# Performance work log

Measured on AMD Instinct MI355X. Metric: run time of the kernel, lower is better.

Reference implementation:

```python
import jax, jax.numpy as jnp
import numpy as np
import math

B, CIN, COUT, K, SD, H, W = 16, 512, 512, 3, 512, 32, 32


def setup_inputs() -> dict:
    key = jax.random.key(0)
    ks = jax.random.split(key, 7)
    return {
        "x": jax.random.normal(ks[0], (B, CIN, H, W), jnp.float32),
        "style": jax.random.normal(ks[1], (B, SD), jnp.float32),
        "noise": jax.random.normal(ks[2], (B, 1, H, W), jnp.float32),
        "weight": jax.random.normal(ks[3], (COUT, CIN, K, K), jnp.float32),
        "mod_w": jax.random.normal(ks[4], (CIN, SD), jnp.float32),
        "mod_b": jnp.ones((CIN,), jnp.float32),
        "noise_weight": jax.random.normal(ks[5], (1,), jnp.float32) * 0.1,
        "act_bias": jax.random.normal(ks[6], (COUT,), jnp.float32) * 0.1,
    }


def reference(x, style, noise, weight, mod_w, mod_b, noise_weight, act_bias):
    conv_scale = 1.0 / math.sqrt(CIN * K * K)  # equalized-lr scale of ModulatedConv2d
    mod_scale = 1.0 / math.sqrt(SD)            # EqualLinear scale (lr_mul=1)

    # style modulation: EqualLinear(style_dim -> in_channel), bias init 1
    s = style @ (mod_w.T * mod_scale) + mod_b              # [B, CIN]

    # per-sample modulated weights [B, COUT, CIN, K, K]
    w = conv_scale * weight[None] * s[:, None, :, None, None]

    # demodulation
    demod = jax.lax.rsqrt(jnp.sum(w * w, axis=(2, 3, 4)) + 1e-8)  # [B, COUT]
    w = w * demod[:, :, None, None, None]

    # grouped (per-sample) conv: vmap a single-sample conv over the batch
    pad = K // 2

    def conv1(xi, wi):
        return jax.lax.conv_general_dilated(
            xi[None], wi, window_strides=(1, 1),
            padding=[(pad, pad), (pad, pad)],
            dimension_numbers=("NCHW", "OIHW", "NCHW"))[0]

    out = jax.vmap(conv1)(x, w)  # [B, COUT, H, W]

    # NoiseInjection: out + weight * noise (scalar learned weight)
    out = out + noise_weight[0] * noise

    # FusedLeakyReLU: leaky_relu(out + bias, 0.2) * sqrt(2)
    out = jax.nn.leaky_relu(out + act_bias[None, :, None, None], 0.2) * math.sqrt(2.0)
    return out
```

## Files before the change

### kernel.cpp

```cpp
#include <hip/hip_runtime.h>
#include <cstdint>
#include <cstddef>

typedef unsigned short u16;
typedef __attribute__((ext_vector_type(8))) short short8;
typedef __attribute__((ext_vector_type(4))) float f32x4;

#define CIN   512
#define COUT  512
#define BATCH 16
#define HWSZ  1024
#define PADW  34

static constexpr float MOD_SCALE  = 0.044194173824159216f;
static constexpr float CONV_SCALE = 0.014731391274719739f;

#define WS_S    0
#define WS_DSC  (32*1024)
#define WS_WSQ  (64*1024)
#define WS_WBT  (64*1024 + 1024*1024)
#define WS_XSP  (WS_WBT + 9*512*512*2)

__device__ __forceinline__ u16 f2bf(float f) {
  union { float f; uint32_t u; } v; v.f = f;
  uint32_t r = v.u + 0x7fffu + ((v.u >> 16) & 1u);
  return (u16)(r >> 16);
}

__device__ __forceinline__ void gload16(const void* g, void* l) {
  __builtin_amdgcn_global_load_lds(
      (const __attribute__((address_space(1))) void*)g,
      (__attribute__((address_space(3))) void*)l, 16, 0, 0);
}

__global__ void k_style(const float* __restrict__ style, const float* __restrict__ mod_w,
                        const float* __restrict__ mod_b, float* __restrict__ s_out) {
  int gid  = blockIdx.x * blockDim.x + threadIdx.x;
  int w    = gid >> 6, lane = gid & 63;
  int b    = w >> 9, i = w & 511;
  const float4* st = (const float4*)(style + (size_t)b * 512);
  const float4* mw = (const float4*)(mod_w + (size_t)i * 512);
  float4 a0 = st[lane * 2], a1 = st[lane * 2 + 1];
  float4 w0 = mw[lane * 2], w1 = mw[lane * 2 + 1];
  float acc = a0.x*w0.x + a0.y*w0.y + a0.z*w0.z + a0.w*w0.w
            + a1.x*w1.x + a1.y*w1.y + a1.z*w1.z + a1.w*w1.w;
  #pragma unroll
  for (int off = 32; off; off >>= 1) acc += __shfl_xor(acc, off);
  if (lane == 0) s_out[w] = acc * MOD_SCALE + mod_b[i];
}

__global__ void k_wprep(const float* __restrict__ w, float* __restrict__ wsq,
                        u16* __restrict__ wbt) {
  int idx = blockIdx.x * 256 + threadIdx.x;
  const float* p = w + (size_t)idx * 9;
  float a = 0.f;
  #pragma unroll
  for (int kxy = 0; kxy < 9; ++kxy) {
    float v = p[kxy];
    a += v * v;
    wbt[(size_t)kxy * 262144 + idx] = f2bf(v);
  }
  wsq[idx] = a;
}

__global__ void k_dscale(const float* __restrict__ wsq, const float* __restrict__ s,
                         float* __restrict__ dsc) {
  int gid  = blockIdx.x * blockDim.x + threadIdx.x;
  int w    = gid >> 6, lane = gid & 63;
  int b    = w >> 9, o = w & 511;
  const float4* q4 = (const float4*)(wsq + (size_t)o * 512);
  const float4* s4 = (const float4*)(s   + (size_t)b * 512);
  float4 q0 = q4[lane * 2], q1 = q4[lane * 2 + 1];
  float4 t0 = s4[lane * 2], t1 = s4[lane * 2 + 1];
  float acc = q0.x*t0.x*t0.x + q0.y*t0.y*t0.y + q0.z*t0.z*t0.z + q0.w*t0.w*t0.w
            + q1.x*t1.x*t1.x + q1.y*t1.y*t1.y + q1.z*t1.z*t1.z + q1.w*t1.w*t1.w;
  #pragma unroll
  for (int off = 32; off; off >>= 1) acc += __shfl_xor(acc, off);
  if (lane == 0)
    dsc[w] = CONV_SCALE * rsqrtf(acc * CONV_SCALE * CONV_SCALE + 1e-8f);
}

__global__ void k_xs(const float* __restrict__ x, const float* __restrict__ s,
                     u16* __restrict__ xsp) {
  __shared__ float tile[64][33];
  int icb = blockIdx.x, y = blockIdx.y, b = blockIdx.z;
  int t = threadIdx.x;
  int i0 = icb * 64;
  int c  = t & 31;
  int r0 = t >> 5;
  #pragma unroll
  for (int it = 0; it < 8; ++it) {
    int row = r0 + it * 8;
    float sv = s[b * 512 + i0 + row];
    tile[row][c] = x[((size_t)(b * 512 + i0 + row)) * 1024 + y * 32 + c] * sv;
  }
  __syncthreads();
  int il = t & 63;
  int x0 = t >> 6;
  #pragma unroll
  for (int it = 0; it < 8; ++it) {
    int xc = x0 + it * 4;
    xsp[((size_t)((b * PADW + y + 1) * PADW) + (xc + 1)) * 512 + i0 + il] = f2bf(tile[il][xc]);
  }
}

__global__ __launch_bounds__(512, 2) void k_conv(
    const u16* __restrict__ wbt, const u16* __restrict__ xsp,
    const float* __restrict__ dsc, const float* __restrict__ noise,
    const float* __restrict__ nw, const float* __restrict__ abias,
    float* __restrict__ out)
{
  __shared__ u16 Ald[3 * 16384];
  __shared__ u16 Bld[3 * 8192];

  const int tid  = threadIdx.x;
  const int wave = tid >> 6, lane = tid & 63;

  const int bid = blockIdx.x;
  const int swz = (bid & 7) * 32 + (bid >> 3);
  const int o0 = (swz >> 7) << 8;
  const int m0 = (swz & 127) << 7;
  const int b  = m0 >> 10;

  const int cc = (((lane & 7) ^ (lane >> 3)) * 8);
  const u16* gA[4]; int lAo[4];
  #pragma unroll
  for (int q = 0; q < 4; ++q) {
    int r = wave * 32 + q * 8 + (lane >> 3);
    gA[q] = wbt + (size_t)(o0 + r) * 512 + cc;
    lAo[q] = (wave * 32 + q * 8) * 64;
  }
  const u16* gB[2]; int lBo[2];
  #pragma unroll
  for (int q = 0; q < 2; ++q) {
    int r = wave * 16 + q * 8 + (lane >> 3);
    int mg = m0 + r;
    int yy = (mg >> 5) & 31, xx = mg & 31;
    gB[q] = xsp + ((size_t)(b * PADW + yy) * PADW + xx) * 512 + cc;
    lBo[q] = (wave * 16 + q * 8) * 64;
  }

  f32x4 acc[4][4];
  #pragma unroll
  for (int i = 0; i < 4; ++i)
    #pragma unroll
    for (int j = 0; j < 4; ++j) acc[i][j] = (f32x4){0.f, 0.f, 0.f, 0.f};

  const int wo = (wave >> 1) * 64;
  const int wm = (wave & 1) * 64;
  const int lrow = lane & 15;
  const int lk   = (lane >> 4) * 8;
  const int rsw  = (lrow & 7) << 3;

  auto stage = [&](int ks, int sa, int sb) {
    int kxy = ks >> 3, ib = (ks & 7) << 6;
    int ky = kxy / 3, kx = kxy - ky * 3;
    int offA = kxy * 262144 + ib;
    int offB = ((ky * PADW + kx) << 9) + ib;
    #pragma unroll
    for (int q = 0; q < 4; ++q) gload16(gA[q] + offA, &Ald[sa + lAo[q]]);
    #pragma unroll
    for (int q = 0; q < 2; ++q) gload16(gB[q] + offB, &Bld[sb + lBo[q]]);
  };

  auto compute = [&](int ca, int cb) {
    #pragma unroll
    for (int kh = 0; kh < 2; ++kh) {
      int kos = (kh * 32 + lk) ^ rsw;
      short8 av[4], bv[4];
      #pragma unroll
      for (int mi = 0; mi < 4; ++mi)
        av[mi] = *(const short8*)&Ald[ca + (wo + mi * 16 + lrow) * 64 + kos];
      #pragma unroll
      for (int ni = 0; ni < 4; ++ni)
        bv[ni] = *(const short8*)&Bld[cb + (wm + ni * 16 + lrow) * 64 + kos];
      #pragma unroll
      for (int mi = 0; mi < 4; ++mi)
        #pragma unroll
        for (int ni = 0; ni < 4; ++ni)
          acc[mi][ni] = __builtin_amdgcn_mfma_f32_16x16x32_bf16(
              av[mi], bv[ni], acc[mi][ni], 0, 0, 0);
    }
  };

  stage(0, 0, 0);
  stage(1, 16384, 8192);

  for (int t = 0; t < 24; ++t) {
    int k0 = t * 3;
    asm volatile("s_waitcnt vmcnt(6)" ::: "memory");
    __builtin_amdgcn_s_barrier();
    if (k0 + 2 < 72) stage(k0 + 2, 32768, 16384);
    compute(0, 0);
    asm volatile("s_waitcnt vmcnt(6)" ::: "memory");
    __builtin_amdgcn_s_barrier();
    if (k0 + 3 < 72) stage(k0 + 3, 0, 0);
    compute(16384, 8192);
    if (k0 + 2 == 71) { asm volatile("s_waitcnt vmcnt(0)" ::: "memory"); }
    else              { asm volatile("s_waitcnt vmcnt(6)" ::: "memory"); }
    __builtin_amdgcn_s_barrier();
    if (k0 + 4 < 72) stage(k0 + 4, 16384, 8192);
    compute(32768, 16384);
  }

  const float nwv = nw[0];
  const int mrow = (lane >> 4) << 2;
  #pragma unroll
  for (int mi = 0; mi < 4; ++mi) {
    #pragma unroll
    for (int ni = 0; ni < 4; ++ni) {
      int mg = m0 + wm + ni * 16 + lrow;
      int hw = mg & 1023;
      float nz = nwv * noise[b * 1024 + hw];
      #pragma unroll
      for (int r = 0; r < 4; ++r) {
        int og = o0 + wo + mi * 16 + mrow + r;
        float v = acc[mi][ni][r] * dsc[b * 512 + og] + nz + abias[og];
        v = (v > 0.f ? v : 0.2f * v) * 1.4142135623730951f;
        out[(size_t)(b * 512 + og) * 1024 + hw] = v;
      }
    }
  }
}

extern "C" void kernel_launch(void* const* d_in, const int* in_sizes, int n_in,
                              void* d_out, int out_size, void* d_ws, size_t ws_size,
                              hipStream_t stream) {
  const float* x      = (const float*)d_in[0];
  const float* style  = (const float*)d_in[1];
  const float* noise  = (const float*)d_in[2];
  const float* weight = (const float*)d_in[3];
  const float* mod_w  = (const float*)d_in[4];
  const float* mod_b  = (const float*)d_in[5];
  const float* nw     = (const float*)d_in[6];
  const float* abias  = (const float*)d_in[7];
  float* out = (float*)d_out;

  char* ws = (char*)d_ws;
  float* s_buf = (float*)(ws + WS_S);
  float* dsc   = (float*)(ws + WS_DSC);
  float* wsq   = (float*)(ws + WS_WSQ);
  u16*   wbt   = (u16*)(ws + WS_WBT);
  u16*   xsp   = (u16*)(ws + WS_XSP);

  hipMemsetAsync(xsp, 0, (size_t)BATCH * PADW * PADW * 512 * 2, stream);

  k_style <<<2048, 256, 0, stream>>>(style, mod_w, mod_b, s_buf);
  k_wprep <<<1024, 256, 0, stream>>>(weight, wsq, wbt);
  k_dscale<<<2048, 256, 0, stream>>>(wsq, s_buf, dsc);
  k_xs    <<<dim3(8, 32, 16), 256, 0, stream>>>(x, s_buf, xsp);
  k_conv  <<<256, 512, 0, stream>>>(wbt, xsp, dsc, noise, nw, abias, out);
}
```

Baseline: 114.7 us.

## Split conv waves into ping-pong groups and zero only padding halo

The main conv kernel now splits its 8 waves into two groups of 4. They alternate K-steps: one group runs MFMAs from registers it preloaded while the other group reads the next LDS tile into registers. Each wave now owns a 128x64 output tile with double register fragments, and setprio is raised around the compute phase. The two groups' partial sums are reduced through shared memory before the epilogue. Separately, the full-buffer memset of the padded activation buffer is replaced by a small kernel that zeroes only the halo cells. This removes a large memset but raises register pressure and adds a reduction step.

```diff
diff --git a/kernel.cpp b/kernel.cpp
--- a/kernel.cpp
+++ b/kernel.cpp
@@ -80,6 +80,18 @@
     dsc[w] = CONV_SCALE * rsqrtf(acc * CONV_SCALE * CONV_SCALE + 1e-8f);
 }
 
+__global__ void k_halo(u16* __restrict__ xsp) {
+  int cell = blockIdx.x;
+  int b = blockIdx.y;
+  int y, x;
+  if (cell < 34)       { y = 0;          x = cell; }
+  else if (cell < 68)  { y = 33;         x = cell - 34; }
+  else if (cell < 100) { y = cell - 67;  x = 0; }
+  else                 { y = cell - 99;  x = 33; }
+  uint32_t* p = (uint32_t*)(xsp + ((size_t)(b * PADW + y) * PADW + x) * 512);
+  p[threadIdx.x] = 0;
+}
+
 __global__ void k_xs(const float* __restrict__ x, const float* __restrict__ s,
                      u16* __restrict__ xsp) {
   __shared__ float tile[64][33];
@@ -110,11 +122,14 @@
     const float* __restrict__ nw, const float* __restrict__ abias,
     float* __restrict__ out)
 {
-  __shared__ u16 Ald[3 * 16384];
-  __shared__ u16 Bld[3 * 8192];
+  __shared__ u16 SM[73728];
 
   const int tid  = threadIdx.x;
   const int wave = tid >> 6, lane = tid & 63;
+  const int grp  = wave >> 2;
+  const int pos  = wave & 3;
+  const int wo = (pos >> 1) * 128;
+  const int wm = (pos & 1) * 64;
 
   const int bid = blockIdx.x;
   const int swz = (bid & 7) * 32 + (bid >> 3);
@@ -140,84 +155,120 @@
     lBo[q] = (wave * 16 + q * 8) * 64;
   }
 
-  f32x4 acc[4][4];
-  #pragma unroll
-  for (int i = 0; i < 4; ++i)
+  f32x4 acc[8][4];
+  #pragma unroll
+  for (int i = 0; i < 8; ++i)
     #pragma unroll
     for (int j = 0; j < 4; ++j) acc[i][j] = (f32x4){0.f, 0.f, 0.f, 0.f};
 
-  const int wo = (wave >> 1) * 64;
-  const int wm = (wave & 1) * 64;
   const int lrow = lane & 15;
   const int lk   = (lane >> 4) * 8;
   const int rsw  = (lrow & 7) << 3;
-
-  auto stage = [&](int ks, int sa, int sb) {
+  const int kos0 = lk ^ rsw;
+  const int kos1 = (32 + lk) ^ rsw;
+
+  short8 avp[2][8], bvp[2][4];
+
+  auto stage = [&](int ks, int bufi) {
+    int sa = bufi * 16384, sb = 49152 + bufi * 8192;
     int kxy = ks >> 3, ib = (ks & 7) << 6;
     int ky = kxy / 3, kx = kxy - ky * 3;
     int offA = kxy * 262144 + ib;
     int offB = ((ky * PADW + kx) << 9) + ib;
     #pragma unroll
-    for (int q = 0; q < 4; ++q) gload16(gA[q] + offA, &Ald[sa + lAo[q]]);
-    #pragma unroll
-    for (int q = 0; q < 2; ++q) gload16(gB[q] + offB, &Bld[sb + lBo[q]]);
+    for (int q = 0; q < 4; ++q) gload16(gA[q] + offA, &SM[sa + lAo[q]]);
+    #pragma unroll
+    for (int q = 0; q < 2; ++q) gload16(gB[q] + offB, &SM[sb + lBo[q]]);
   };
 
-  auto compute = [&](int ca, int cb) {
-    #pragma unroll
-    for (int kh = 0; kh < 2; ++kh) {
-      int kos = (kh * 32 + lk) ^ rsw;
-      short8 av[4], bv[4];
+  auto preread = [&](int bufi) {
+    int ca = bufi * 16384, cb = 49152 + bufi * 8192;
+    #pragma unroll
+    for (int mi = 0; mi < 8; ++mi) {
+      avp[0][mi] = *(const short8*)&SM[ca + (wo + mi * 16 + lrow) * 64 + kos0];
+      avp[1][mi] = *(const short8*)&SM[ca + (wo + mi * 16 + lrow) * 64 + kos1];
+    }
+    #pragma unroll
+    for (int ni = 0; ni < 4; ++ni) {
+      bvp[0][ni] = *(const short8*)&SM[cb + (wm + ni * 16 + lrow) * 64 + kos0];
+      bvp[1][ni] = *(const short8*)&SM[cb + (wm + ni * 16 + lrow) * 64 + kos1];
+    }
+  };
+
+  auto compute = [&]() {
+    __builtin_amdgcn_s_setprio(1);
+    #pragma unroll
+    for (int kh = 0; kh < 2; ++kh)
       #pragma unroll
-      for (int mi = 0; mi < 4; ++mi)
-        av[mi] = *(const short8*)&Ald[ca + (wo + mi * 16 + lrow) * 64 + kos];
-      #pragma unroll
-      for (int ni = 0; ni < 4; ++ni)
-        bv[ni] = *(const short8*)&Bld[cb + (wm + ni * 16 + lrow) * 64 + kos];
-      #pragma unroll
-      for (int mi = 0; mi < 4; ++mi)
+      for (int mi = 0; mi < 8; ++mi)
         #pragma unroll
         for (int ni = 0; ni < 4; ++ni)
           acc[mi][ni] = __builtin_amdgcn_mfma_f32_16x16x32_bf16(
-              av[mi], bv[ni], acc[mi][ni], 0, 0, 0);
-    }
+              avp[kh][mi], bvp[kh][ni], acc[mi][ni], 0, 0, 0);
+    __builtin_amdgcn_s_setprio(0);
   };
 
-  stage(0, 0, 0);
-  stage(1, 16384, 8192);
-
-  for (int t = 0; t < 24; ++t) {
-    int k0 = t * 3;
-    asm volatile("s_waitcnt vmcnt(6)" ::: "memory");
-    __builtin_amdgcn_s_barrier();
-    if (k0 + 2 < 72) stage(k0 + 2, 32768, 16384);
-    compute(0, 0);
-    asm volatile("s_waitcnt vmcnt(6)" ::: "memory");
-    __builtin_amdgcn_s_barrier();
-    if (k0 + 3 < 72) stage(k0 + 3, 0, 0);
-    compute(16384, 8192);
-    if (k0 + 2 == 71) { asm volatile("s_waitcnt vmcnt(0)" ::: "memory"); }
-    else              { asm volatile("s_waitcnt vmcnt(6)" ::: "memory"); }
-    __builtin_amdgcn_s_barrier();
-    if (k0 + 4 < 72) stage(k0 + 4, 16384, 8192);
-    compute(32768, 16384);
-  }
-
-  const float nwv = nw[0];
-  const int mrow = (lane >> 4) << 2;
-  #pragma unroll
-  for (int mi = 0; mi < 4; ++mi) {
-    #pragma unroll
-    for (int ni = 0; ni < 4; ++ni) {
-      int mg = m0 + wm + ni * 16 + lrow;
-      int hw = mg & 1023;
-      float nz = nwv * noise[b * 1024 + hw];
+  stage(0, 0);
+  stage(1, 1);
+  asm volatile("s_waitcnt vmcnt(6)" ::: "memory");
+  __builtin_amdgcn_s_barrier();
+  if (grp == 0) preread(0);
+
+#define STEP(KS, BPRE, BNXT, WN, DOSTAGE, PREOK)                         \
+  {                                                                      \
+    if (DOSTAGE) stage((KS) + 2, BNXT);                                  \
+    asm volatile("s_waitcnt vmcnt(" #WN ")" ::: "memory");               \
+    __builtin_amdgcn_s_barrier();                                        \
+    if (grp == ((KS) & 1)) compute();                                    \
+    else if (PREOK) preread(BPRE);                                       \
+  }
+
+  for (int t = 0; t < 11; ++t) {
+    const int k0 = t * 6;
+    STEP(k0 + 0, 1, 2, 6, 1, 1);
+    STEP(k0 + 1, 2, 0, 6, 1, 1);
+    STEP(k0 + 2, 0, 1, 6, 1, 1);
+    STEP(k0 + 3, 1, 2, 6, 1, 1);
+    STEP(k0 + 4, 2, 0, 6, 1, 1);
+    STEP(k0 + 5, 0, 1, 6, 1, 1);
+  }
+  STEP(66, 1, 2, 6, 1, 1);
+  STEP(67, 2, 0, 6, 1, 1);
+  STEP(68, 0, 1, 6, 1, 1);
+  STEP(69, 1, 2, 6, 1, 1);
+  STEP(70, 2, 0, 0, 0, 1);
+  STEP(71, 0, 1, 0, 0, 0);
+#undef STEP
+
+  float* red = (float*)SM;
+  __syncthreads();
+  if (grp == 1) {
+    #pragma unroll
+    for (int mi = 0; mi < 8; ++mi)
       #pragma unroll
-      for (int r = 0; r < 4; ++r) {
-        int og = o0 + wo + mi * 16 + mrow + r;
-        float v = acc[mi][ni][r] * dsc[b * 512 + og] + nz + abias[og];
-        v = (v > 0.f ? v : 0.2f * v) * 1.4142135623730951f;
-        out[(size_t)(b * 512 + og) * 1024 + hw] = v;
+      for (int ni = 0; ni < 4; ++ni)
+        *(f32x4*)&red[pos * 8192 + (mi * 4 + ni) * 256 + lane * 4] = acc[mi][ni];
+  }
+  __syncthreads();
+  if (grp == 0) {
+    const float nwv = nw[0];
+    const int mrow = (lane >> 4) << 2;
+    #pragma unroll
+    for (int mi = 0; mi < 8; ++mi) {
+      #pragma unroll
+      for (int ni = 0; ni < 4; ++ni) {
+        f32x4 other = *(const f32x4*)&red[pos * 8192 + (mi * 4 + ni) * 256 + lane * 4];
+        f32x4 a = acc[mi][ni] + other;
+        int mg = m0 + wm + ni * 16 + lrow;
+        int hw = mg & 1023;
+        float nz = nwv * noise[b * 1024 + hw];
+        #pragma unroll
+        for (int r = 0; r < 4; ++r) {
+          int og = o0 + wo + mi * 16 + mrow + r;
+          float v = a[r] * dsc[b * 512 + og] + nz + abias[og];
+          v = (v > 0.f ? v : 0.2f * v) * 1.4142135623730951f;
+          out[(size_t)(b * 512 + og) * 1024 + hw] = v;
+        }
       }
     }
   }
@@ -243,8 +294,7 @@
   u16*   wbt   = (u16*)(ws + WS_WBT);
   u16*   xsp   = (u16*)(ws + WS_XSP);
 
-  hipMemsetAsync(xsp, 0, (size_t)BATCH * PADW * PADW * 512 * 2, stream);
-
+  k_halo  <<<dim3(132, 16), 256, 0, stream>>>(xsp);
   k_style <<<2048, 256, 0, stream>>>(style, mod_w, mod_b, s_buf);
   k_wprep <<<1024, 256, 0, stream>>>(weight, wsq, wbt);
   k_dscale<<<2048, 256, 0, stream>>>(wsq, s_buf, dsc);
```

New measurement: 201.3 us. +75.5%, slower.

## Load weight fragments straight to registers and zero only the halo

Applied to the files above, without the earlier changes.

Weights are repacked into an MFMA-fragment-friendly layout so each lane loads its A operands directly from global memory into registers, double-buffered one k-step ahead. This drops the LDS staging buffer for A and its reads. The B pipeline is unrolled into a 6-step macro with sched barriers and raised wave priority around the MFMAs. The full memset of the padded input is replaced by a small kernel that zeroes only the border cells. The cost is more registers and global-load latency exposed directly to the register file.

```diff
diff --git a/kernel.cpp b/kernel.cpp
--- a/kernel.cpp
+++ b/kernel.cpp
@@ -50,15 +50,16 @@
 }
 
 __global__ void k_wprep(const float* __restrict__ w, float* __restrict__ wsq,
-                        u16* __restrict__ wbt) {
+                        u16* __restrict__ wbt2) {
   int idx = blockIdx.x * 256 + threadIdx.x;
+  int o = idx >> 9, i = idx & 511;
   const float* p = w + (size_t)idx * 9;
   float a = 0.f;
   #pragma unroll
   for (int kxy = 0; kxy < 9; ++kxy) {
     float v = p[kxy];
     a += v * v;
-    wbt[(size_t)kxy * 262144 + idx] = f2bf(v);
+    wbt2[((size_t)(kxy * 64 + (i >> 3)) * 512 + o) * 8 + (i & 7)] = f2bf(v);
   }
   wsq[idx] = a;
 }
@@ -80,6 +81,18 @@
     dsc[w] = CONV_SCALE * rsqrtf(acc * CONV_SCALE * CONV_SCALE + 1e-8f);
 }
 
+__global__ void k_halo(u16* __restrict__ xsp) {
+  int cell = blockIdx.x;
+  int b = blockIdx.y;
+  int y, x;
+  if (cell < 34)       { y = 0;          x = cell; }
+  else if (cell < 68)  { y = 33;         x = cell - 34; }
+  else if (cell < 100) { y = cell - 67;  x = 0; }
+  else                 { y = cell - 99;  x = 33; }
+  uint32_t* p = (uint32_t*)(xsp + ((size_t)(b * PADW + y) * PADW + x) * 512);
+  p[threadIdx.x] = 0;
+}
+
 __global__ void k_xs(const float* __restrict__ x, const float* __restrict__ s,
                      u16* __restrict__ xsp) {
   __shared__ float tile[64][33];
@@ -105,12 +118,11 @@
 }
 
 __global__ __launch_bounds__(512, 2) void k_conv(
-    const u16* __restrict__ wbt, const u16* __restrict__ xsp,
+    const u16* __restrict__ wbt2, const u16* __restrict__ xsp,
     const float* __restrict__ dsc, const float* __restrict__ noise,
     const float* __restrict__ nw, const float* __restrict__ abias,
     float* __restrict__ out)
 {
-  __shared__ u16 Ald[3 * 16384];
   __shared__ u16 Bld[3 * 8192];
 
   const int tid  = threadIdx.x;
@@ -122,14 +134,15 @@
   const int m0 = (swz & 127) << 7;
   const int b  = m0 >> 10;
 
+  const int wo = (wave >> 1) * 64;
+  const int wm = (wave & 1) * 64;
+  const int lrow = lane & 15;
+  const int lk   = (lane >> 4) * 8;
+  const int rsw  = (lrow & 7) << 3;
+
+  const u16* pA = wbt2 + (size_t)(lane >> 4) * 4096 + (size_t)(o0 + wo + lrow) * 8;
+
   const int cc = (((lane & 7) ^ (lane >> 3)) * 8);
-  const u16* gA[4]; int lAo[4];
-  #pragma unroll
-  for (int q = 0; q < 4; ++q) {
-    int r = wave * 32 + q * 8 + (lane >> 3);
-    gA[q] = wbt + (size_t)(o0 + r) * 512 + cc;
-    lAo[q] = (wave * 32 + q * 8) * 64;
-  }
   const u16* gB[2]; int lBo[2];
   #pragma unroll
   for (int q = 0; q < 2; ++q) {
@@ -146,31 +159,33 @@
     #pragma unroll
     for (int j = 0; j < 4; ++j) acc[i][j] = (f32x4){0.f, 0.f, 0.f, 0.f};
 
-  const int wo = (wave >> 1) * 64;
-  const int wm = (wave & 1) * 64;
-  const int lrow = lane & 15;
-  const int lk   = (lane >> 4) * 8;
-  const int rsw  = (lrow & 7) << 3;
-
-  auto stage = [&](int ks, int sa, int sb) {
+  short8 av0[2][4], av1[2][4];
+
+  auto avload = [&](int ks, short8 (&dst)[2][4]) {
+    const u16* base = pA + (size_t)(ks >> 3) * 262144 + (size_t)(ks & 7) * 32768;
+    #pragma unroll
+    for (int kh = 0; kh < 2; ++kh)
+      #pragma unroll
+      for (int mi = 0; mi < 4; ++mi)
+        dst[kh][mi] = *(const short8*)(base + kh * 16384 + mi * 128);
+  };
+
+  auto stageB = [&](int ks, int bufi) {
     int kxy = ks >> 3, ib = (ks & 7) << 6;
     int ky = kxy / 3, kx = kxy - ky * 3;
-    int offA = kxy * 262144 + ib;
     int offB = ((ky * PADW + kx) << 9) + ib;
-    #pragma unroll
-    for (int q = 0; q < 4; ++q) gload16(gA[q] + offA, &Ald[sa + lAo[q]]);
+    int sb = bufi * 8192;
     #pragma unroll
     for (int q = 0; q < 2; ++q) gload16(gB[q] + offB, &Bld[sb + lBo[q]]);
   };
 
-  auto compute = [&](int ca, int cb) {
+  auto compute = [&](const short8 (&av)[2][4], int bufi) {
+    const int cb = bufi * 8192;
+    __builtin_amdgcn_s_setprio(1);
     #pragma unroll
     for (int kh = 0; kh < 2; ++kh) {
       int kos = (kh * 32 + lk) ^ rsw;
-      short8 av[4], bv[4];
-      #pragma unroll
-      for (int mi = 0; mi < 4; ++mi)
-        av[mi] = *(const short8*)&Ald[ca + (wo + mi * 16 + lrow) * 64 + kos];
+      short8 bv[4];
       #pragma unroll
       for (int ni = 0; ni < 4; ++ni)
         bv[ni] = *(const short8*)&Bld[cb + (wm + ni * 16 + lrow) * 64 + kos];
@@ -179,29 +194,42 @@
         #pragma unroll
         for (int ni = 0; ni < 4; ++ni)
           acc[mi][ni] = __builtin_amdgcn_mfma_f32_16x16x32_bf16(
-              av[mi], bv[ni], acc[mi][ni], 0, 0, 0);
+              av[kh][mi], bv[ni], acc[mi][ni], 0, 0, 0);
     }
+    __builtin_amdgcn_s_setprio(0);
   };
 
-  stage(0, 0, 0);
-  stage(1, 16384, 8192);
-
-  for (int t = 0; t < 24; ++t) {
-    int k0 = t * 3;
-    asm volatile("s_waitcnt vmcnt(6)" ::: "memory");
-    __builtin_amdgcn_s_barrier();
-    if (k0 + 2 < 72) stage(k0 + 2, 32768, 16384);
-    compute(0, 0);
-    asm volatile("s_waitcnt vmcnt(6)" ::: "memory");
-    __builtin_amdgcn_s_barrier();
-    if (k0 + 3 < 72) stage(k0 + 3, 0, 0);
-    compute(16384, 8192);
-    if (k0 + 2 == 71) { asm volatile("s_waitcnt vmcnt(0)" ::: "memory"); }
-    else              { asm volatile("s_waitcnt vmcnt(6)" ::: "memory"); }
-    __builtin_amdgcn_s_barrier();
-    if (k0 + 4 < 72) stage(k0 + 4, 16384, 8192);
-    compute(32768, 16384);
-  }
+  stageB(0, 0);
+  stageB(1, 1);
+  avload(0, av0);
+
+#define STEP(KS, AVCUR, AVNXT, BBUF, BNXT, DOAV, DOSTAGE, WN)            \
+  {                                                                      \
+    if (DOAV) avload((KS) + 1, AVNXT);                                   \
+    __builtin_amdgcn_sched_barrier(0);                                   \
+    asm volatile("s_waitcnt vmcnt(" #WN ")" ::: "memory");               \
+    __builtin_amdgcn_s_barrier();                                        \
+    __builtin_amdgcn_sched_barrier(0);                                   \
+    if (DOSTAGE) stageB((KS) + 2, BNXT);                                 \
+    compute(AVCUR, BBUF);                                                \
+  }
+
+  for (int t = 0; t < 11; ++t) {
+    const int k0 = t * 6;
+    STEP(k0 + 0, av0, av1, 0, 2, 1, 1, 8);
+    STEP(k0 + 1, av1, av0, 1, 0, 1, 1, 8);
+    STEP(k0 + 2, av0, av1, 2, 1, 1, 1, 8);
+    STEP(k0 + 3, av1, av0, 0, 2, 1, 1, 8);
+    STEP(k0 + 4, av0, av1, 1, 0, 1, 1, 8);
+    STEP(k0 + 5, av1, av0, 2, 1, 1, 1, 8);
+  }
+  STEP(66, av0, av1, 0, 2, 1, 1, 8);
+  STEP(67, av1, av0, 1, 0, 1, 1, 8);
+  STEP(68, av0, av1, 2, 1, 1, 1, 8);
+  STEP(69, av1, av0, 0, 2, 1, 1, 8);
+  STEP(70, av0, av1, 1, 0, 1, 0, 8);
+  STEP(71, av1, av0, 2, 1, 0, 0, 0);
+#undef STEP
 
   const float nwv = nw[0];
   const int mrow = (lane >> 4) << 2;
@@ -240,14 +268,13 @@
   float* s_buf = (float*)(ws + WS_S);
   float* dsc   = (float*)(ws + WS_DSC);
   float* wsq   = (float*)(ws + WS_WSQ);
-  u16*   wbt   = (u16*)(ws + WS_WBT);
+  u16*   wbt2  = (u16*)(ws + WS_WBT);
   u16*   xsp   = (u16*)(ws + WS_XSP);
 
-  hipMemsetAsync(xsp, 0, (size_t)BATCH * PADW * PADW * 512 * 2, stream);
-
+  k_halo  <<<dim3(132, 16), 256, 0, stream>>>(xsp);
   k_style <<<2048, 256, 0, stream>>>(style, mod_w, mod_b, s_buf);
-  k_wprep <<<1024, 256, 0, stream>>>(weight, wsq, wbt);
+  k_wprep <<<1024, 256, 0, stream>>>(weight, wsq, wbt2);
   k_dscale<<<2048, 256, 0, stream>>>(wsq, s_buf, dsc);
   k_xs    <<<dim3(8, 32, 16), 256, 0, stream>>>(x, s_buf, xsp);
-  k_conv  <<<256, 512, 0, stream>>>(wbt, xsp, dsc, noise, nw, abias, out);
-}
+  k_conv  <<<256, 512, 0, stream>>>(wbt2, xsp, dsc, noise, nw, abias, out);
+}
```

After: 105.2 us. 1.09x faster.

## Interleave LDS reads, staged loads and prioritized MFMA phases; zero only halo

Applied to the files above, without the earlier changes.

The conv main loop is split into four sub-phases per k-tile. Each phase issues a slice of the global-to-LDS prefetch, brackets its MFMA group with barriers and s_setprio, and loads fewer A fragments at a time, so memory traffic overlaps with matrix math across waves. Launch bounds change to one block per CU. A small kernel that writes zeros only to the padding border replaces the full memset of the padded input buffer. The extra barriers could add synchronisation overhead, and the lower occupancy hint could reduce latency hiding.

```diff
diff --git a/kernel.cpp b/kernel.cpp
--- a/kernel.cpp
+++ b/kernel.cpp
@@ -80,6 +80,18 @@
     dsc[w] = CONV_SCALE * rsqrtf(acc * CONV_SCALE * CONV_SCALE + 1e-8f);
 }
 
+__global__ void k_halo(u16* __restrict__ xsp) {
+  int cell = blockIdx.x;
+  int b = blockIdx.y;
+  int y, x;
+  if (cell < 34)       { y = 0;          x = cell; }
+  else if (cell < 68)  { y = 33;         x = cell - 34; }
+  else if (cell < 100) { y = cell - 67;  x = 0; }
+  else                 { y = cell - 99;  x = 33; }
+  uint32_t* p = (uint32_t*)(xsp + ((size_t)(b * PADW + y) * PADW + x) * 512);
+  p[threadIdx.x] = 0;
+}
+
 __global__ void k_xs(const float* __restrict__ x, const float* __restrict__ s,
                      u16* __restrict__ xsp) {
   __shared__ float tile[64][33];
@@ -104,7 +116,7 @@
   }
 }
 
-__global__ __launch_bounds__(512, 2) void k_conv(
+__global__ __launch_bounds__(512, 1) void k_conv(
     const u16* __restrict__ wbt, const u16* __restrict__ xsp,
     const float* __restrict__ dsc, const float* __restrict__ noise,
     const float* __restrict__ nw, const float* __restrict__ abias,
@@ -122,6 +134,14 @@
   const int m0 = (swz & 127) << 7;
   const int b  = m0 >> 10;
 
+  const int wo = (wave >> 1) * 64;
+  const int wm = (wave & 1) * 64;
+  const int lrow = lane & 15;
+  const int lk   = (lane >> 4) * 8;
+  const int rsw  = (lrow & 7) << 3;
+  const int kos0 = lk ^ rsw;
+  const int kos1 = (32 + lk) ^ rsw;
+
   const int cc = (((lane & 7) ^ (lane >> 3)) * 8);
   const u16* gA[4]; int lAo[4];
   #pragma unroll
@@ -146,62 +166,92 @@
     #pragma unroll
     for (int j = 0; j < 4; ++j) acc[i][j] = (f32x4){0.f, 0.f, 0.f, 0.f};
 
-  const int wo = (wave >> 1) * 64;
-  const int wm = (wave & 1) * 64;
-  const int lrow = lane & 15;
-  const int lk   = (lane >> 4) * 8;
-  const int rsw  = (lrow & 7) << 3;
-
-  auto stage = [&](int ks, int sa, int sb) {
+  auto stgA = [&](int ks, int bufi, int q0) {
+    int kxy = ks >> 3, ib = (ks & 7) << 6;
+    int offA = kxy * 262144 + ib;
+    gload16(gA[q0] + offA,     &Ald[bufi * 16384 + lAo[q0]]);
+    gload16(gA[q0 + 1] + offA, &Ald[bufi * 16384 + lAo[q0 + 1]]);
+  };
+  auto stgB = [&](int ks, int bufi) {
     int kxy = ks >> 3, ib = (ks & 7) << 6;
     int ky = kxy / 3, kx = kxy - ky * 3;
-    int offA = kxy * 262144 + ib;
     int offB = ((ky * PADW + kx) << 9) + ib;
-    #pragma unroll
-    for (int q = 0; q < 4; ++q) gload16(gA[q] + offA, &Ald[sa + lAo[q]]);
-    #pragma unroll
-    for (int q = 0; q < 2; ++q) gload16(gB[q] + offB, &Bld[sb + lBo[q]]);
+    gload16(gB[0] + offB, &Bld[bufi * 8192 + lBo[0]]);
+    gload16(gB[1] + offB, &Bld[bufi * 8192 + lBo[1]]);
   };
 
-  auto compute = [&](int ca, int cb) {
-    #pragma unroll
-    for (int kh = 0; kh < 2; ++kh) {
-      int kos = (kh * 32 + lk) ^ rsw;
-      short8 av[4], bv[4];
-      #pragma unroll
-      for (int mi = 0; mi < 4; ++mi)
-        av[mi] = *(const short8*)&Ald[ca + (wo + mi * 16 + lrow) * 64 + kos];
-      #pragma unroll
-      for (int ni = 0; ni < 4; ++ni)
-        bv[ni] = *(const short8*)&Bld[cb + (wm + ni * 16 + lrow) * 64 + kos];
-      #pragma unroll
-      for (int mi = 0; mi < 4; ++mi)
-        #pragma unroll
-        for (int ni = 0; ni < 4; ++ni)
-          acc[mi][ni] = __builtin_amdgcn_mfma_f32_16x16x32_bf16(
-              av[mi], bv[ni], acc[mi][ni], 0, 0, 0);
+#define LDA(CA, MI, KOS) (*(const short8*)&Ald[(CA) + (wo + (MI) * 16 + lrow) * 64 + (KOS)])
+#define LDB(CB, NI, KOS) (*(const short8*)&Bld[(CB) + (wm + (NI) * 16 + lrow) * 64 + (KOS)])
+
+#define MFMA8(MI0)                                                        \
+    _Pragma("unroll")                                                     \
+    for (int ni = 0; ni < 4; ++ni) {                                      \
+      acc[(MI0)][ni] = __builtin_amdgcn_mfma_f32_16x16x32_bf16(           \
+          av0, bv[ni], acc[(MI0)][ni], 0, 0, 0);                          \
+      acc[(MI0) + 1][ni] = __builtin_amdgcn_mfma_f32_16x16x32_bf16(       \
+          av1, bv[ni], acc[(MI0) + 1][ni], 0, 0, 0);                      \
     }
-  };
-
-  stage(0, 0, 0);
-  stage(1, 16384, 8192);
-
-  for (int t = 0; t < 24; ++t) {
-    int k0 = t * 3;
-    asm volatile("s_waitcnt vmcnt(6)" ::: "memory");
-    __builtin_amdgcn_s_barrier();
-    if (k0 + 2 < 72) stage(k0 + 2, 32768, 16384);
-    compute(0, 0);
-    asm volatile("s_waitcnt vmcnt(6)" ::: "memory");
-    __builtin_amdgcn_s_barrier();
-    if (k0 + 3 < 72) stage(k0 + 3, 0, 0);
-    compute(16384, 8192);
-    if (k0 + 2 == 71) { asm volatile("s_waitcnt vmcnt(0)" ::: "memory"); }
-    else              { asm volatile("s_waitcnt vmcnt(6)" ::: "memory"); }
-    __builtin_amdgcn_s_barrier();
-    if (k0 + 4 < 72) stage(k0 + 4, 16384, 8192);
-    compute(32768, 16384);
-  }
+
+#define KTILE(CUR, NXT, KS2, DOSTG, VM)                                   \
+  {                                                                       \
+    const int ca = (CUR) * 16384, cb = (CUR) * 8192;                      \
+    short8 av0, av1, bv[4];                                               \
+                                                \
+    av0 = LDA(ca, 0, kos0); av1 = LDA(ca, 1, kos0);                       \
+    bv[0] = LDB(cb, 0, kos0); bv[1] = LDB(cb, 1, kos0);                   \
+    bv[2] = LDB(cb, 2, kos0); bv[3] = LDB(cb, 3, kos0);                   \
+    if (DOSTG) stgA(KS2, NXT, 0);                                         \
+    __builtin_amdgcn_s_barrier();                                         \
+    __builtin_amdgcn_s_setprio(1);                                        \
+    MFMA8(0);                                                             \
+    __builtin_amdgcn_s_setprio(0);                                        \
+    __builtin_amdgcn_s_barrier();                                         \
+                                    \
+    av0 = LDA(ca, 2, kos0); av1 = LDA(ca, 3, kos0);                       \
+    if (DOSTG) stgA(KS2, NXT, 2);                                         \
+    __builtin_amdgcn_s_barrier();                                         \
+    __builtin_amdgcn_s_setprio(1);                                        \
+    MFMA8(2);                                                             \
+    __builtin_amdgcn_s_setprio(0);                                        \
+    __builtin_amdgcn_s_barrier();                                         \
+                                                \
+    av0 = LDA(ca, 0, kos1); av1 = LDA(ca, 1, kos1);                       \
+    bv[0] = LDB(cb, 0, kos1); bv[1] = LDB(cb, 1, kos1);                   \
+    bv[2] = LDB(cb, 2, kos1); bv[3] = LDB(cb, 3, kos1);                   \
+    if (DOSTG) stgB(KS2, NXT);                                            \
+    __builtin_amdgcn_s_barrier();                                         \
+    __builtin_amdgcn_s_setprio(1);                                        \
+    MFMA8(0);                                                             \
+    __builtin_amdgcn_s_setprio(0);                                        \
+    __builtin_amdgcn_s_barrier();                                         \
+                 \
+    av0 = LDA(ca, 2, kos1); av1 = LDA(ca, 3, kos1);                       \
+    __builtin_amdgcn_s_barrier();                                         \
+    __builtin_amdgcn_s_setprio(1);                                        \
+    MFMA8(2);                                                             \
+    __builtin_amdgcn_s_setprio(0);                                        \
+    asm volatile("s_waitcnt vmcnt(" #VM ")" ::: "memory");                \
+    __builtin_amdgcn_s_barrier();                                         \
+  }
+
+  stgA(0, 0, 0); stgA(0, 0, 2); stgB(0, 0);
+  stgA(1, 1, 0); stgA(1, 1, 2); stgB(1, 1);
+  asm volatile("s_waitcnt vmcnt(6)" ::: "memory");
+  __builtin_amdgcn_s_barrier();
+
+  for (int t = 0; t < 23; ++t) {
+    const int k0 = t * 3;
+    KTILE(0, 2, k0 + 2, 1, 6);
+    KTILE(1, 0, k0 + 3, 1, 6);
+    KTILE(2, 1, k0 + 4, 1, 6);
+  }
+  KTILE(0, 2, 71, 1, 6);
+  KTILE(1, 0, 0, 0, 0);
+  KTILE(2, 1, 0, 0, 0);
+#undef KTILE
+#undef MFMA8
+#undef LDA
+#undef LDB
 
   const float nwv = nw[0];
   const int mrow = (lane >> 4) << 2;
@@ -243,8 +293,7 @@
   u16*   wbt   = (u16*)(ws + WS_WBT);
   u16*   xsp   = (u16*)(ws + WS_XSP);
 
-  hipMemsetAsync(xsp, 0, (size_t)BATCH * PADW * PADW * 512 * 2, stream);
-
+  k_halo  <<<dim3(132, 16), 256, 0, stream>>>(xsp);
   k_style <<<2048, 256, 0, stream>>>(style, mod_w, mod_b, s_buf);
   k_wprep <<<1024, 256, 0, stream>>>(weight, wsq, wbt);
   k_dscale<<<2048, 256, 0, stream>>>(wsq, s_buf, dsc);
```

Measured after the change: 133.0 us. 15.9% more time.
